# Kernel tuning notes

Hardware: AMD Instinct MI355X
Metric: run time of the kernel (lower is better)

Reference implementation:

```python
import jax, jax.numpy as jnp
import numpy as np

K = 3                # k_const
NUM_CLASSES = 10
CLASS_SIZE = 5000
NUM_TRAIN = NUM_CLASSES * CLASS_SIZE   # 50000
DIGIT_WIDTH = 256
NUM_TEST = 4096


def setup_inputs() -> dict:
    key = jax.random.key(0)
    k1, k2 = jax.random.split(key)
    training_set = jax.random.randint(k1, (NUM_TRAIN, DIGIT_WIDTH), 0, 2, dtype=jnp.int32)
    test_set = jax.random.randint(k2, (NUM_TEST, DIGIT_WIDTH), 0, 2, dtype=jnp.int32)
    return {"training_set": training_set, "test_set": test_set}


def reference(training_set, test_set):
    # Hamming distance between binary vectors a,b: sum(a XOR b)
    # = sum(a) + sum(b) - 2*dot(a,b); computed as one int matmul instead of
    # materializing the [T, N, D] XOR tensor.
    tr_sum = jnp.sum(training_set, axis=1)                    # [N]
    te_sum = jnp.sum(test_set, axis=1)                        # [T]
    inner = jnp.matmul(test_set, training_set.T)              # [T, N] int32
    dists = te_sum[:, None] + tr_sum[None, :] - 2 * inner     # [T, N]

    # Original loop keeps the K smallest distances, ties won by the earlier
    # training index (strict '<' insertion). lax.top_k on negated distances
    # breaks ties by smaller index, matching that behavior.
    _, knn_idx = jax.lax.top_k(-dists, K)                     # [T, K]
    labels = knn_idx // CLASS_SIZE                            # [T, K]

    # Majority vote per test sample; argmax returns first max on ties,
    # same as torch.argmax in the original.
    T = test_set.shape[0]
    votes = jnp.zeros((T, NUM_CLASSES), dtype=jnp.int32)
    votes = votes.at[jnp.arange(T)[:, None], labels].add(1)   # [T, C]
    return jnp.argmax(votes, axis=1)                          # [T]
```

## Files before the change

### kernel.cpp

```cpp
#include <hip/hip_runtime.h>
#include <stdint.h>

typedef unsigned long long u64;
typedef unsigned int u32;
typedef int v4i  __attribute__((ext_vector_type(4)));
typedef int v16i __attribute__((ext_vector_type(16)));

#define NUM_TRAIN   50000
#define NUM_TEST    4096
#define CLASS_SIZE  5000
#define TRAIN_PAD   50176
#define TOT_TILES   1568

#define SZ_TRAIN   ((size_t)TRAIN_PAD * 256)
#define SZ_TEST    ((size_t)NUM_TEST * 256)
#define SZ_TESUM   ((size_t)NUM_TEST * 4)
#define OFF_TEST   (SZ_TRAIN)
#define OFF_TESUM  (OFF_TEST + SZ_TEST)
#define OFF_PART   (OFF_TESUM + SZ_TESUM)
#define WS_NEED(NCH) (OFF_PART + (size_t)NUM_TEST * (NCH) * 3 * 4)

__device__ __forceinline__ void insert3(u32& k0, u32& k1, u32& k2, u32 key) {
    u32 m1, m2;
    asm("v_med3_u32 %0, %1, %2, %3" : "=v"(m1) : "v"(k0), "v"(k1), "v"(key));
    asm("v_med3_u32 %0, %1, %2, %3" : "=v"(m2) : "v"(k1), "v"(k2), "v"(key));
    k0 = min(k0, key);
    k1 = m1; k2 = m2;
}
__device__ __forceinline__ void merge3(u32& a0, u32& a1, u32& a2,
                                       u32 b0, u32 b1, u32 b2) {
    u32 hi0 = max(a0, b0);
    u32 lo1 = min(a1, b1);
    u32 c0  = min(a0, b0);
    u32 c1  = min(hi0, lo1);
    u32 c2  = min(max(lo1, hi0), min(a2, b2));
    a0 = c0; a1 = c1; a2 = c2;
}
__device__ __forceinline__ int wave_sum(int s) {
    #pragma unroll
    for (int off = 1; off < 64; off <<= 1) s += __shfl_xor(s, off);
    return s;
}
__device__ __forceinline__ void gload16(const void* g, void* l) {
    __builtin_amdgcn_global_load_lds(
        (const __attribute__((address_space(1))) unsigned int*)g,
        (__attribute__((address_space(3))) unsigned int*)l, 16, 0, 0);
}

__global__ __launch_bounds__(256) void pack_all(const int* __restrict__ train,
                                                const int* __restrict__ test,
                                                char* __restrict__ dstA,
                                                char* __restrict__ dstB,
                                                int* __restrict__ tesum) {
    int r    = (blockIdx.x * 256 + threadIdx.x) >> 6;
    int lane = threadIdx.x & 63;
    if (r < TRAIN_PAD) {
        int4 v = make_int4(0, 0, 0, 0);
        if (r < NUM_TRAIN)
            v = *reinterpret_cast<const int4*>(train + (size_t)r * 256 + lane * 4);
        u32 w = (u32)(v.x & 1) | ((u32)(v.y & 1) << 8)
              | ((u32)(v.z & 1) << 16) | ((u32)(v.w & 1) << 24);
        const int tile = r >> 5, row = r & 31;
        const int kk   = lane >> 3;
        const int kh   = (lane >> 2) & 1;
        const int slot = (row ^ kk) & 31;
        size_t dst = (size_t)tile * 8192 + kk * 1024 + kh * 512
                   + (size_t)slot * 16 + (lane & 3) * 4;
        *reinterpret_cast<u32*>(dstA + dst) = w;
    } else {
        int rt = r - TRAIN_PAD;
        int4 v = *reinterpret_cast<const int4*>(test + (size_t)rt * 256 + lane * 4);
        u32 w = (u32)((1 - 2 * v.x) & 0xFF) | ((u32)((1 - 2 * v.y) & 0xFF) << 8)
              | ((u32)((1 - 2 * v.z) & 0xFF) << 16) | ((u32)((1 - 2 * v.w) & 0xFF) << 24);
        *reinterpret_cast<u32*>(dstB + (size_t)rt * 256 + lane * 4) = w;
        int total = wave_sum(v.x + v.y + v.z + v.w);
        if (lane == 0) tesum[rt] = total;
    }
}

template<int NCH>
__global__ __launch_bounds__(256) void mfma_knn(const char* __restrict__ A,
                                                const char* __restrict__ Bt,
                                                const int* __restrict__ tesum,
                                                u32* __restrict__ partial) {
    constexpr int TILES  = TOT_TILES / NCH;
    constexpr int CHROWS = TRAIN_PAD / NCH;
    static_assert((TILES & 1) == 0, "2-phase dbuf loop needs even TILES");
    static_assert((CHROWS & 31) == 0, "chunk must be whole tiles");
    const int cg   = blockIdx.x / NCH;
    const int c    = blockIdx.x % NCH;
    const int tid  = threadIdx.x;
    const int wid  = tid >> 6;
    const int lane = tid & 63;
    const int a    = lane & 31;
    const int kh   = lane >> 5;

    const int col0 = cg * 256 + wid * 64 + a;
    const int col1 = col0 + 32;
    v4i bf0[8], bf1[8];
    {
        const char* bp0 = Bt + (size_t)col0 * 256 + kh * 16;
        const char* bp1 = Bt + (size_t)col1 * 256 + kh * 16;
        #pragma unroll
        for (int kk = 0; kk < 8; ++kk) {
            bf0[kk] = *reinterpret_cast<const v4i*>(bp0 + kk * 32);
            bf1[kk] = *reinterpret_cast<const v4i*>(bp1 + kk * 32);
        }
    }
    const u32 base0 = ((u32)tesum[col0] << 16);
    const u32 base1 = ((u32)tesum[col1] << 16);

    __shared__ char lds[2][8192];
    char* rd[8];
    #pragma unroll
    for (int kk = 0; kk < 8; ++kk)
        rd[kk] = &lds[0][kk * 1024 + kh * 512 + ((a ^ kk) & 31) * 16];

    const char* asrc = A + (size_t)(c * (CHROWS / 32)) * 8192
                         + wid * 2048 + lane * 16;

    u32 p00 = 0x7FFFFFFFu, p01 = 0x7FFFFFFFu, p02 = 0x7FFFFFFFu;
    u32 p10 = 0x7FFFFFFFu, p11 = 0x7FFFFFFFu, p12 = 0x7FFFFFFFu;

    gload16(asrc,        &lds[0][wid * 2048]);
    gload16(asrc + 1024, &lds[0][wid * 2048 + 1024]);
    __syncthreads();

#define TILE_STEP(TT, RB, WB)                                                 \
    {                                                                         \
        const int tt = (TT);                                                  \
        if (tt + 1 < TILES) {                                                 \
            const char* g = asrc + (size_t)(tt + 1) * 8192;                   \
            gload16(g,        &lds[WB][wid * 2048]);                          \
            gload16(g + 1024, &lds[WB][wid * 2048 + 1024]);                   \
        }                                                                     \
        v16i acc0 = {0,0,0,0,0,0,0,0,0,0,0,0,0,0,0,0};                        \
        v16i acc1 = {0,0,0,0,0,0,0,0,0,0,0,0,0,0,0,0};                        \
        __builtin_amdgcn_s_setprio(1);                                        \
        _Pragma("unroll")                                                     \
        for (int kk = 0; kk < 8; ++kk) {                                      \
            v4i af = *reinterpret_cast<const v4i*>(rd[kk] + (RB) * 8192);     \
            acc0 = __builtin_amdgcn_mfma_i32_32x32x32_i8(af, bf0[kk], acc0, 0, 0, 0); \
            acc1 = __builtin_amdgcn_mfma_i32_32x32x32_i8(af, bf1[kk], acc1, 0, 0, 0); \
        }                                                                     \
        __builtin_amdgcn_s_setprio(0);                                        \
        const int tbase = c * CHROWS + tt * 32;                               \
        const u32 kb0 = base0 + (u32)(tbase + 4 * kh);                        \
        const u32 kb1 = base1 + (u32)(tbase + 4 * kh);                        \
        if (tbase + 32 <= NUM_TRAIN) {                                        \
            _Pragma("unroll")                                                 \
            for (int g = 0; g < 16; ++g) {                                    \
                const int row = (g & 3) + 8 * (g >> 2);                       \
                insert3(p00, p01, p02, ((u32)acc0[g] << 16) + kb0 + (u32)row);\
                insert3(p10, p11, p12, ((u32)acc1[g] << 16) + kb1 + (u32)row);\
            }                                                                 \
        } else {                                                              \
            _Pragma("unroll")                                                 \
            for (int g = 0; g < 16; ++g) {                                    \
                const int row = (g & 3) + 8 * (g >> 2);                       \
                const int idx = tbase + 4 * kh + row;                         \
                u32 key0 = (idx < NUM_TRAIN)                                  \
                    ? (((u32)acc0[g] << 16) + kb0 + (u32)row) : 0xFFFFFFFFu;  \
                u32 key1 = (idx < NUM_TRAIN)                                  \
                    ? (((u32)acc1[g] << 16) + kb1 + (u32)row) : 0xFFFFFFFFu;  \
                insert3(p00, p01, p02, key0);                                 \
                insert3(p10, p11, p12, key1);                                 \
            }                                                                 \
        }                                                                     \
        __syncthreads();                                                      \
    }

    #pragma unroll 1
    for (int t = 0; t < TILES; t += 2) {
        TILE_STEP(t,     0, 1);
        TILE_STEP(t + 1, 1, 0);
    }
#undef TILE_STEP

    u32 o0, o1, o2;
    o0 = __shfl_xor(p00, 32); o1 = __shfl_xor(p01, 32); o2 = __shfl_xor(p02, 32);
    merge3(p00, p01, p02, o0, o1, o2);
    o0 = __shfl_xor(p10, 32); o1 = __shfl_xor(p11, 32); o2 = __shfl_xor(p12, 32);
    merge3(p10, p11, p12, o0, o1, o2);
    if (kh == 0) {
        u32* d0 = partial + ((size_t)c * NUM_TEST + col0) * 3;
        d0[0] = p00; d0[1] = p01; d0[2] = p02;
        u32* d1 = partial + ((size_t)c * NUM_TEST + col1) * 3;
        d1[0] = p10; d1[1] = p11; d1[2] = p12;
    }
}

template<int NCH>
__global__ __launch_bounds__(256) void vote_knn(const u32* __restrict__ partial,
                                                int* __restrict__ out) {
    int t = blockIdx.x * 256 + threadIdx.x;
    if (t >= NUM_TEST) return;
    const u32* p0 = partial + (size_t)t * 3;
    u32 a0 = p0[0], a1 = p0[1], a2 = p0[2];
    #pragma unroll 8
    for (int c = 1; c < NCH; ++c) {
        const u32* q = partial + ((size_t)c * NUM_TEST + t) * 3;
        merge3(a0, a1, a2, q[0], q[1], q[2]);
    }
    const int l0 = (int)(a0 & 0xFFFFu) / CLASS_SIZE;
    const int l1 = (int)(a1 & 0xFFFFu) / CLASS_SIZE;
    const int l2 = (int)(a2 & 0xFFFFu) / CLASS_SIZE;
    int winner;
    if (l0 == l1 || l0 == l2)      winner = l0;
    else if (l1 == l2)             winner = l1;
    else winner = min(l0, min(l1, l2));
    out[t] = winner;
}

#define TT          8
#define NCHUNK      4
#define CHUNK_ROWS  (NUM_TRAIN / NCHUNK)

__device__ __forceinline__ void insert3_minmax(u32& k0, u32& k1, u32& k2, u32 key) {
    u32 m0 = min(k0, key);
    u32 m1 = min(k1, max(k0, key));
    u32 m2 = min(k2, max(k1, key));
    k0 = m0; k1 = m1; k2 = m2;
}

__global__ void pack_kernel(const int* __restrict__ train,
                            const int* __restrict__ test,
                            u64* __restrict__ packed) {
    int wave = (blockIdx.x * blockDim.x + threadIdx.x) >> 6;
    int lane = threadIdx.x & 63;
    const int* src = (wave < NUM_TRAIN)
                       ? (train + (size_t)wave * 256)
                       : (test + (size_t)(wave - NUM_TRAIN) * 256);
    int4 v = *reinterpret_cast<const int4*>(src + lane * 4);
    u64 b0 = __ballot(v.x & 1);
    u64 b1 = __ballot(v.y & 1);
    u64 b2 = __ballot(v.z & 1);
    u64 b3 = __ballot(v.w & 1);
    if (lane == 0) {
        u64* dst = packed + (size_t)wave * 4;
        dst[0] = b0; dst[1] = b1; dst[2] = b2; dst[3] = b3;
    }
}

__global__ __launch_bounds__(256) void knn_kernel(const u32* __restrict__ packed,
                                                  u32* __restrict__ partial) {
    const int g    = blockIdx.x >> 2;
    const int c    = blockIdx.x & 3;
    const int tid  = threadIdx.x;
    const int base = g * TT;
    const uint4* rows  = (const uint4*)packed;
    const u32*  testp  = packed + (size_t)NUM_TRAIN * 8;

    u32 te[TT][8];
    #pragma unroll
    for (int s = 0; s < TT; ++s) {
        const u32* p = testp + (size_t)(base + s) * 8;
        #pragma unroll
        for (int j = 0; j < 8; ++j) te[s][j] = p[j];
    }
    u32 k0[TT], k1[TT], k2[TT];
    #pragma unroll
    for (int s = 0; s < TT; ++s) { k0[s] = k1[s] = k2[s] = 0x7FFFFFFFu; }

    const int start = c * CHUNK_ROWS;
    const int end   = start + CHUNK_ROWS;
    for (int r = start + tid; r < end; r += 256) {
        uint4 a0 = rows[(size_t)r * 2];
        uint4 a1 = rows[(size_t)r * 2 + 1];
        #pragma unroll
        for (int s = 0; s < TT; ++s) {
            int d = __popc(a0.x ^ te[s][0]);
            d += __popc(a0.y ^ te[s][1]);
            d += __popc(a0.z ^ te[s][2]);
            d += __popc(a0.w ^ te[s][3]);
            d += __popc(a1.x ^ te[s][4]);
            d += __popc(a1.y ^ te[s][5]);
            d += __popc(a1.z ^ te[s][6]);
            d += __popc(a1.w ^ te[s][7]);
            u32 key = ((u32)d << 16) | (u32)r;
            insert3_minmax(k0[s], k1[s], k2[s], key);
        }
    }
    #pragma unroll
    for (int s = 0; s < TT; ++s) {
        for (int off = 1; off < 64; off <<= 1) {
            u32 o0 = __shfl_xor(k0[s], off);
            u32 o1 = __shfl_xor(k1[s], off);
            u32 o2 = __shfl_xor(k2[s], off);
            merge3(k0[s], k1[s], k2[s], o0, o1, o2);
        }
    }
    __shared__ u32 red[4][TT][3];
    const int wave = tid >> 6, lane = tid & 63;
    if (lane == 0) {
        #pragma unroll
        for (int s = 0; s < TT; ++s) {
            red[wave][s][0] = k0[s];
            red[wave][s][1] = k1[s];
            red[wave][s][2] = k2[s];
        }
    }
    __syncthreads();
    if (tid < TT) {
        const int s = tid;
        u32 a0 = red[0][s][0], a1 = red[0][s][1], a2 = red[0][s][2];
        #pragma unroll
        for (int w = 1; w < 4; ++w)
            merge3(a0, a1, a2, red[w][s][0], red[w][s][1], red[w][s][2]);
        u32* dst = partial + ((size_t)(base + s) * NCHUNK + c) * 3;
        dst[0] = a0; dst[1] = a1; dst[2] = a2;
    }
}

__global__ __launch_bounds__(256) void merge_kernel(const u32* __restrict__ partial,
                                                    int* __restrict__ out) {
    int t = blockIdx.x * blockDim.x + threadIdx.x;
    if (t >= NUM_TEST) return;
    const u32* p = partial + (size_t)t * NCHUNK * 3;
    u32 a0 = p[0], a1 = p[1], a2 = p[2];
    #pragma unroll
    for (int c = 1; c < NCHUNK; ++c)
        merge3(a0, a1, a2, p[c * 3 + 0], p[c * 3 + 1], p[c * 3 + 2]);
    const int l0 = (int)(a0 & 0xFFFFu) / CLASS_SIZE;
    const int l1 = (int)(a1 & 0xFFFFu) / CLASS_SIZE;
    const int l2 = (int)(a2 & 0xFFFFu) / CLASS_SIZE;
    int winner;
    if (l0 == l1 || l0 == l2)      winner = l0;
    else if (l1 == l2)             winner = l1;
    else winner = min(l0, min(l1, l2));
    out[t] = winner;
}

extern "C" void kernel_launch(void* const* d_in, const int* in_sizes, int n_in,
                              void* d_out, int out_size, void* d_ws, size_t ws_size,
                              hipStream_t stream) {
    const int* train = (const int*)d_in[0];
    const int* test  = (const int*)d_in[1];
    int* out = (int*)d_out;

    if (ws_size >= WS_NEED(112)) {
        char* train_swz = (char*)d_ws;
        char* test_i8   = (char*)d_ws + OFF_TEST;
        int*  tesum     = (int*)((char*)d_ws + OFF_TESUM);
        u32*  partial   = (u32*)((char*)d_ws + OFF_PART);

        pack_all<<<(TRAIN_PAD + NUM_TEST) / 4, 256, 0, stream>>>(train, test,
                                                                 train_swz, test_i8, tesum);
        mfma_knn<112><<<16 * 112, 256, 0, stream>>>(train_swz, test_i8, tesum, partial);
        vote_knn<112><<<NUM_TEST / 256, 256, 0, stream>>>(partial, out);
    } else {
        u64* packed = (u64*)d_ws;
        u32* partial = (u32*)((char*)d_ws + (size_t)(NUM_TRAIN + NUM_TEST) * 4 * sizeof(u64));
        const int total_rows = NUM_TRAIN + NUM_TEST;
        pack_kernel<<<total_rows / 4, 256, 0, stream>>>(train, test, packed);
        knn_kernel<<<(NUM_TEST / TT) * NCHUNK, 256, 0, stream>>>((const u32*)packed, partial);
        merge_kernel<<<(NUM_TEST + 255) / 256, 256, 0, stream>>>(partial, out);
    }
}
```

Baseline: 92.79 us.

## Triple-buffer LDS tile loads and parallelize chunk merge across 16 lanes

The MFMA kNN kernel moves from a double-buffered LDS loop with a full __syncthreads per tile to a three-buffer ring. Loads are issued two tiles ahead, with explicit vmcnt waits and raw barriers, so global-to-LDS latency is hidden behind more compute. The vote kernel now spreads the 112 chunk partials for each test sample across 16 lanes and reduces them with shuffle merges, instead of running one serial 112-step loop per thread. The cost is 50% more LDS per block, which may lower occupancy, and the change depends on gload16 being counted by vmcnt in the expected order.

```diff
diff --git a/kernel.cpp b/kernel.cpp
--- a/kernel.cpp
+++ b/kernel.cpp
@@ -85,7 +85,6 @@
                                                 u32* __restrict__ partial) {
     constexpr int TILES  = TOT_TILES / NCH;
     constexpr int CHROWS = TRAIN_PAD / NCH;
-    static_assert((TILES & 1) == 0, "2-phase dbuf loop needs even TILES");
     static_assert((CHROWS & 31) == 0, "chunk must be whole tiles");
     const int cg   = blockIdx.x / NCH;
     const int c    = blockIdx.x % NCH;
@@ -110,7 +109,7 @@
     const u32 base0 = ((u32)tesum[col0] << 16);
     const u32 base1 = ((u32)tesum[col1] << 16);
 
-    __shared__ char lds[2][8192];
+    __shared__ char lds[3][8192];
     char* rd[8];
     #pragma unroll
     for (int kk = 0; kk < 8; ++kk)
@@ -118,64 +117,70 @@
 
     const char* asrc = A + (size_t)(c * (CHROWS / 32)) * 8192
                          + wid * 2048 + lane * 16;
+    char* ldst = &lds[0][wid * 2048];
 
     u32 p00 = 0x7FFFFFFFu, p01 = 0x7FFFFFFFu, p02 = 0x7FFFFFFFu;
     u32 p10 = 0x7FFFFFFFu, p11 = 0x7FFFFFFFu, p12 = 0x7FFFFFFFu;
 
-    gload16(asrc,        &lds[0][wid * 2048]);
-    gload16(asrc + 1024, &lds[0][wid * 2048 + 1024]);
-    __syncthreads();
-
-#define TILE_STEP(TT, RB, WB)                                                 \
-    {                                                                         \
-        const int tt = (TT);                                                  \
-        if (tt + 1 < TILES) {                                                 \
-            const char* g = asrc + (size_t)(tt + 1) * 8192;                   \
-            gload16(g,        &lds[WB][wid * 2048]);                          \
-            gload16(g + 1024, &lds[WB][wid * 2048 + 1024]);                   \
-        }                                                                     \
-        v16i acc0 = {0,0,0,0,0,0,0,0,0,0,0,0,0,0,0,0};                        \
-        v16i acc1 = {0,0,0,0,0,0,0,0,0,0,0,0,0,0,0,0};                        \
-        __builtin_amdgcn_s_setprio(1);                                        \
-        _Pragma("unroll")                                                     \
-        for (int kk = 0; kk < 8; ++kk) {                                      \
-            v4i af = *reinterpret_cast<const v4i*>(rd[kk] + (RB) * 8192);     \
-            acc0 = __builtin_amdgcn_mfma_i32_32x32x32_i8(af, bf0[kk], acc0, 0, 0, 0); \
-            acc1 = __builtin_amdgcn_mfma_i32_32x32x32_i8(af, bf1[kk], acc1, 0, 0, 0); \
-        }                                                                     \
-        __builtin_amdgcn_s_setprio(0);                                        \
-        const int tbase = c * CHROWS + tt * 32;                               \
-        const u32 kb0 = base0 + (u32)(tbase + 4 * kh);                        \
-        const u32 kb1 = base1 + (u32)(tbase + 4 * kh);                        \
-        if (tbase + 32 <= NUM_TRAIN) {                                        \
-            _Pragma("unroll")                                                 \
-            for (int g = 0; g < 16; ++g) {                                    \
-                const int row = (g & 3) + 8 * (g >> 2);                       \
-                insert3(p00, p01, p02, ((u32)acc0[g] << 16) + kb0 + (u32)row);\
-                insert3(p10, p11, p12, ((u32)acc1[g] << 16) + kb1 + (u32)row);\
-            }                                                                 \
-        } else {                                                              \
-            _Pragma("unroll")                                                 \
-            for (int g = 0; g < 16; ++g) {                                    \
-                const int row = (g & 3) + 8 * (g >> 2);                       \
-                const int idx = tbase + 4 * kh + row;                         \
-                u32 key0 = (idx < NUM_TRAIN)                                  \
-                    ? (((u32)acc0[g] << 16) + kb0 + (u32)row) : 0xFFFFFFFFu;  \
-                u32 key1 = (idx < NUM_TRAIN)                                  \
-                    ? (((u32)acc1[g] << 16) + kb1 + (u32)row) : 0xFFFFFFFFu;  \
-                insert3(p00, p01, p02, key0);                                 \
-                insert3(p10, p11, p12, key1);                                 \
-            }                                                                 \
-        }                                                                     \
-        __syncthreads();                                                      \
-    }
+    gload16(asrc,                &lds[0][wid * 2048]);
+    gload16(asrc + 1024,         &lds[0][wid * 2048 + 1024]);
+    gload16(asrc + 8192,         &lds[1][wid * 2048]);
+    gload16(asrc + 8192 + 1024,  &lds[1][wid * 2048 + 1024]);
+    asm volatile("s_waitcnt vmcnt(2)" ::: "memory");
+    __builtin_amdgcn_s_barrier();
+
+    u32 roff = 0;
+    u32 woff = 16384;
 
     #pragma unroll 1
-    for (int t = 0; t < TILES; t += 2) {
-        TILE_STEP(t,     0, 1);
-        TILE_STEP(t + 1, 1, 0);
-    }
-#undef TILE_STEP
+    for (int t = 0; t < TILES; ++t) {
+        const bool issue = (t + 2 < TILES);
+        if (issue) {
+            const char* g = asrc + (size_t)(t + 2) * 8192;
+            gload16(g,        ldst + woff);
+            gload16(g + 1024, ldst + woff + 1024);
+        }
+        v16i acc0 = {0,0,0,0,0,0,0,0,0,0,0,0,0,0,0,0};
+        v16i acc1 = {0,0,0,0,0,0,0,0,0,0,0,0,0,0,0,0};
+        __builtin_amdgcn_s_setprio(1);
+        #pragma unroll
+        for (int kk = 0; kk < 8; ++kk) {
+            v4i af = *reinterpret_cast<const v4i*>(rd[kk] + roff);
+            acc0 = __builtin_amdgcn_mfma_i32_32x32x32_i8(af, bf0[kk], acc0, 0, 0, 0);
+            acc1 = __builtin_amdgcn_mfma_i32_32x32x32_i8(af, bf1[kk], acc1, 0, 0, 0);
+        }
+        __builtin_amdgcn_s_setprio(0);
+        const int tbase = c * CHROWS + t * 32;
+        const u32 kb0 = base0 + (u32)(tbase + 4 * kh);
+        const u32 kb1 = base1 + (u32)(tbase + 4 * kh);
+        if (tbase + 32 <= NUM_TRAIN) {
+            #pragma unroll
+            for (int g = 0; g < 16; ++g) {
+                const int row = (g & 3) + 8 * (g >> 2);
+                insert3(p00, p01, p02, ((u32)acc0[g] << 16) + kb0 + (u32)row);
+                insert3(p10, p11, p12, ((u32)acc1[g] << 16) + kb1 + (u32)row);
+            }
+        } else {
+            #pragma unroll
+            for (int g = 0; g < 16; ++g) {
+                const int row = (g & 3) + 8 * (g >> 2);
+                const int idx = tbase + 4 * kh + row;
+                u32 key0 = (idx < NUM_TRAIN)
+                             ? (((u32)acc0[g] << 16) + kb0 + (u32)row) : 0xFFFFFFFFu;
+                u32 key1 = (idx < NUM_TRAIN)
+                             ? (((u32)acc1[g] << 16) + kb1 + (u32)row) : 0xFFFFFFFFu;
+                insert3(p00, p01, p02, key0);
+                insert3(p10, p11, p12, key1);
+            }
+        }
+        if (t + 1 < TILES) {
+            if (issue) asm volatile("s_waitcnt vmcnt(2)" ::: "memory");
+            else       asm volatile("s_waitcnt vmcnt(0)" ::: "memory");
+            __builtin_amdgcn_s_barrier();
+        }
+        roff = (roff == 16384) ? 0 : roff + 8192;
+        woff = (woff == 16384) ? 0 : woff + 8192;
+    }
 
     u32 o0, o1, o2;
     o0 = __shfl_xor(p00, 32); o1 = __shfl_xor(p01, 32); o2 = __shfl_xor(p02, 32);
@@ -191,25 +196,37 @@
 }
 
 template<int NCH>
-__global__ __launch_bounds__(256) void vote_knn(const u32* __restrict__ partial,
-                                                int* __restrict__ out) {
-    int t = blockIdx.x * 256 + threadIdx.x;
+__global__ __launch_bounds__(256) void vote_knn16(const u32* __restrict__ partial,
+                                                  int* __restrict__ out) {
+    static_assert(NCH % 16 == 0, "16-lane vote needs NCH % 16 == 0");
+    const int gid = blockIdx.x * 256 + threadIdx.x;
+    const int t   = gid >> 4;
+    const int sub = gid & 15;
     if (t >= NUM_TEST) return;
-    const u32* p0 = partial + (size_t)t * 3;
-    u32 a0 = p0[0], a1 = p0[1], a2 = p0[2];
-    #pragma unroll 8
-    for (int c = 1; c < NCH; ++c) {
+    u32 a0 = 0x7FFFFFFFu, a1 = 0x7FFFFFFFu, a2 = 0x7FFFFFFFu;
+    #pragma unroll
+    for (int j = 0; j < NCH / 16; ++j) {
+        const int c = sub + 16 * j;
         const u32* q = partial + ((size_t)c * NUM_TEST + t) * 3;
         merge3(a0, a1, a2, q[0], q[1], q[2]);
     }
-    const int l0 = (int)(a0 & 0xFFFFu) / CLASS_SIZE;
-    const int l1 = (int)(a1 & 0xFFFFu) / CLASS_SIZE;
-    const int l2 = (int)(a2 & 0xFFFFu) / CLASS_SIZE;
-    int winner;
-    if (l0 == l1 || l0 == l2)      winner = l0;
-    else if (l1 == l2)             winner = l1;
-    else winner = min(l0, min(l1, l2));
-    out[t] = winner;
+    #pragma unroll
+    for (int off = 1; off < 16; off <<= 1) {
+        u32 o0 = __shfl_xor(a0, off);
+        u32 o1 = __shfl_xor(a1, off);
+        u32 o2 = __shfl_xor(a2, off);
+        merge3(a0, a1, a2, o0, o1, o2);
+    }
+    if (sub == 0) {
+        const int l0 = (int)(a0 & 0xFFFFu) / CLASS_SIZE;
+        const int l1 = (int)(a1 & 0xFFFFu) / CLASS_SIZE;
+        const int l2 = (int)(a2 & 0xFFFFu) / CLASS_SIZE;
+        int winner;
+        if (l0 == l1 || l0 == l2)      winner = l0;
+        else if (l1 == l2)             winner = l1;
+        else winner = min(l0, min(l1, l2));
+        out[t] = winner;
+    }
 }
 
 #define TT          8
@@ -347,7 +364,7 @@
         pack_all<<<(TRAIN_PAD + NUM_TEST) / 4, 256, 0, stream>>>(train, test,
                                                                  train_swz, test_i8, tesum);
         mfma_knn<112><<<16 * 112, 256, 0, stream>>>(train_swz, test_i8, tesum, partial);
-        vote_knn<112><<<NUM_TEST / 256, 256, 0, stream>>>(partial, out);
+        vote_knn16<112><<<(NUM_TEST * 16) / 256, 256, 0, stream>>>(partial, out);
     } else {
         u64* packed = (u64*)d_ws;
         u32* partial = (u32*)((char*)d_ws + (size_t)(NUM_TRAIN + NUM_TEST) * 4 * sizeof(u64));
```

Result: faster. 79.81 us (-14.0%).
